# Kernel tuning notes

Hardware: AMD Instinct MI355X
Metric: run time of the kernel (lower is better)

The kernel has to match this reference:

```python
import jax, jax.numpy as jnp
import numpy as np

N_NODES = 122880  # 4096 graphs * 30 nodes
N_EDGES = 983040


def gcn_conv(x, W, b, src, dst, n):
    """PyG GCNConv: symmetric-normalized aggregation with self-loops."""
    h = x @ W  # [n, out]
    loop = jnp.arange(n, dtype=src.dtype)
    s = jnp.concatenate([src, loop])
    d = jnp.concatenate([dst, loop])
    deg = jnp.zeros((n,), dtype=h.dtype).at[d].add(1.0)  # >=1 due to self loops
    dinv = jax.lax.rsqrt(deg)
    norm = dinv[s] * dinv[d]  # [E+n]
    out = jax.ops.segment_sum(h[s] * norm[:, None], d, num_segments=n)
    return out + b


def setup_inputs() -> dict:
    key = jax.random.key(0)
    ks = jax.random.split(key, 8)
    x = jax.random.normal(ks[0], (N_NODES, 64), dtype=jnp.float32)
    edge_index = jax.random.randint(ks[1], (2, N_EDGES), 0, N_NODES, dtype=jnp.int64)
    W1 = jax.random.normal(ks[2], (64, 128), dtype=jnp.float32) * (1.0 / np.sqrt(64))
    b1 = jnp.zeros((128,), dtype=jnp.float32)
    W2 = jax.random.normal(ks[3], (128, 64), dtype=jnp.float32) * (1.0 / np.sqrt(128))
    b2 = jnp.zeros((64,), dtype=jnp.float32)
    Wfc = jax.random.normal(ks[4], (1920, 1728), dtype=jnp.float32) * (1.0 / np.sqrt(1920))
    bfc = jnp.zeros((1728,), dtype=jnp.float32)
    return {"x": x, "edge_index": edge_index, "W1": W1, "b1": b1,
            "W2": W2, "b2": b2, "Wfc": Wfc, "bfc": bfc}


def reference(x, edge_index, W1, b1, W2, b2, Wfc, bfc):
    n = x.shape[0]
    src, dst = edge_index[0], edge_index[1]
    h = gcn_conv(x, W1, b1, src, dst, n)
    h = jax.nn.relu(h)  # dropout is identity in eval mode
    h = gcn_conv(h, W2, b2, src, dst, n)
    h = jax.nn.relu(h)
    h = h.reshape(-1, 64 * 30)  # [B, 1920], 30 nodes per graph
    return h @ Wfc + bfc  # [B, 1728]
```

## Files before the change

kernel.cpp:

```cpp
#include <hip/hip_runtime.h>
#include <hip/hip_bf16.h>

#define N_NODES 122880
#define N_EDGES 983040
#define NBKT 480
#define BCAP 2560
#define EPB 4096
#define NPAD 1792

typedef __hip_bfloat16 bf16;
typedef __attribute__((ext_vector_type(8))) short short8;
typedef __attribute__((ext_vector_type(4))) float floatx4;

__device__ __forceinline__ void gl_lds16(const void* g, void* l) {
    __builtin_amdgcn_global_load_lds(
        (const __attribute__((address_space(1))) void*)g,
        (__attribute__((address_space(3))) void*)l, 16, 0, 0);
}

__device__ __forceinline__ float bflo(unsigned u) {
    return __uint_as_float(u << 16);
}
__device__ __forceinline__ float bfhi(unsigned u) {
    return __uint_as_float(u & 0xffff0000u);
}

__global__ __launch_bounds__(256) void k_psort_prep(
        const int* __restrict__ ei, int* __restrict__ gcur,
        unsigned* __restrict__ gbuf,
        const float* __restrict__ W1, const float* __restrict__ W2,
        const float* __restrict__ Wfc,
        bf16* __restrict__ W1T, bf16* __restrict__ W2T,
        bf16* __restrict__ WfcT) {
    __shared__ __align__(16) char smem[4352];
    const int b = blockIdx.x, t = threadIdx.x;
    if (b < 240) {
        int* cur = (int*)smem;
        int* gb  = (int*)(smem + 1920);
        for (int i = t; i < NBKT; i += 256) cur[i] = 0;
        __syncthreads();
        const int base = b * EPB;
        unsigned pay[16];
        short bk[16], pib[16];
#pragma unroll
        for (int j = 0; j < 16; ++j) {
            int e = base + j * 256 + t;
            int d = ei[N_EDGES + e];
            int s = ei[e];
            bk[j] = (short)(d >> 8);
            pay[j] = (unsigned)(d & 255) | ((unsigned)s << 8);
            pib[j] = (short)atomicAdd(&cur[d >> 8], 1);
        }
        __syncthreads();
        for (int i = t; i < NBKT; i += 256) {
            int c = cur[i];
            gb[i] = c ? atomicAdd(&gcur[i * 16], c) : 0;
        }
        __syncthreads();
#pragma unroll
        for (int j = 0; j < 16; ++j) {
            int pos = gb[bk[j]] + pib[j];
            if (pos < BCAP) gbuf[bk[j] * BCAP + pos] = pay[j];
        }
    } else if (b < 304) {
        int u = (b - 240) * 256 + t;
        if (u < 64 * 128) {
            int k = u >> 7, n = u & 127;
            W1T[n * 64 + k] = __float2bfloat16(W1[u]);
        } else {
            int v = u - 64 * 128;
            int k = v >> 6, n = v & 63;
            W2T[n * 128 + k] = __float2bfloat16(W2[v]);
        }
    } else {
        float (*ts)[33] = (float(*)[33])smem;
        const int bid2 = b - 304;
        const int n0 = (bid2 % 56) * 32, k0 = (bid2 / 56) * 32;
        const int tx = t & 31, ty = t >> 5;
        const bool nok = (n0 + tx) < 1728;
#pragma unroll
        for (int j = 0; j < 4; ++j)
            ts[ty + j * 8][tx] =
                nok ? Wfc[(long)(k0 + ty + j * 8) * 1728 + n0 + tx] : 0.0f;
        __syncthreads();
#pragma unroll
        for (int j = 0; j < 4; ++j)
            WfcT[(long)(n0 + ty + j * 8) * 1920 + k0 + tx] =
                __float2bfloat16(ts[tx][ty + j * 8]);
    }
}

__global__ __launch_bounds__(256) void k_bcsr(const int* __restrict__ gcur,
                                              const unsigned* __restrict__ gbuf,
                                              int* __restrict__ adj,
                                              unsigned* __restrict__ co,
                                              float* __restrict__ dinv,
                                              const float* __restrict__ x,
                                              bf16* __restrict__ xb) {
    __shared__ int hist[256];
    __shared__ int arr[256];
    __shared__ int exc[256];
    __shared__ float dinvs[256];
    const int b = blockIdx.x, t = threadIdx.x;
    hist[t] = 0;
    __syncthreads();
    int E = gcur[b * 16];
    if (E > BCAP) E = BCAP;
    int dl[10], sv[10];
    short pb[10];
    int n = 0;
    for (int idx = t; idx < E; idx += 256) {
        unsigned p = gbuf[b * BCAP + idx];
        dl[n] = p & 255;
        sv[n] = (int)(p >> 8);
        pb[n] = (short)atomicAdd(&hist[dl[n]], 1);
        ++n;
    }
    __syncthreads();
    const int cnt_t = hist[t];
    arr[t] = cnt_t;
    __syncthreads();
    for (int d = 1; d < 256; d <<= 1) {
        int v = (t >= d) ? arr[t - d] : 0;
        __syncthreads();
        arr[t] += v;
        __syncthreads();
    }
    const int ex = arr[t] - cnt_t;
    exc[t] = ex;
    const int node = b * 256 + t;
    co[node] = ((unsigned)ex << 16) | (unsigned)cnt_t;
    const float di = rsqrtf((float)cnt_t + 1.0f);
    dinv[node] = di;
    dinvs[t] = di;
    __syncthreads();
    for (int j = 0; j < n; ++j)
        adj[b * BCAP + exc[dl[j]] + pb[j]] = sv[j];

    const long xbase = (long)b * 256 * 64;
    for (int r = 0; r < 16; ++r) {
        int u = r * 256 + t;
        int nl = u >> 4;
        const float4 v = ((const float4*)(x + xbase))[u];
        const float d2 = dinvs[nl];
        bf16* o = xb + xbase + u * 4;
        o[0] = __float2bfloat16(d2 * v.x);
        o[1] = __float2bfloat16(d2 * v.y);
        o[2] = __float2bfloat16(d2 * v.z);
        o[3] = __float2bfloat16(d2 * v.w);
    }
}

template <bool BIAS_RELU>
__global__ __launch_bounds__(256) void k_agg(const bf16* __restrict__ xb,
                                             const float* __restrict__ dinv,
                                             const unsigned* __restrict__ co,
                                             const int* __restrict__ adj,
                                             const float* __restrict__ bias,
                                             bf16* __restrict__ out) {
    const int wave = threadIdx.x >> 6, lane = threadIdx.x & 63;
    const int sub = lane >> 4, l16 = lane & 15;
    const int node = blockIdx.x * 16 + wave * 4 + sub;

    const float di = dinv[node];
    const unsigned c_ = co[node];
    int c = (int)(c_ & 0xffffu);
    if (c > 32) c = 32;
    const int* al = adj + (node >> 8) * BCAP + (c_ >> 16);
    int sl  = (l16 < c)      ? al[l16]      : 0;
    int sl2 = (16 + l16 < c) ? al[16 + l16] : 0;

    const uint2 us = *(const uint2*)(xb + ((long)node << 6) + (l16 << 2));
    float a0 = bflo(us.x), a1 = bfhi(us.x);
    float a2 = bflo(us.y), a3 = bfhi(us.y);

    for (int p0 = 0; p0 < c; p0 += 8) {
        uint2 uu[8];
#pragma unroll
        for (int j = 0; j < 8; ++j) {
            int p = p0 + j;
            bool ok = p < c;
            int sv = (p < 16) ? sl : sl2;
            int s = __shfl(sv, p & 15, 16);
            uint2 u = *(const uint2*)(xb + ((long)s << 6) + (l16 << 2));
            uu[j].x = ok ? u.x : 0u;
            uu[j].y = ok ? u.y : 0u;
        }
#pragma unroll
        for (int j = 0; j < 8; ++j) {
            a0 += bflo(uu[j].x);
            a1 += bfhi(uu[j].x);
            a2 += bflo(uu[j].y);
            a3 += bfhi(uu[j].y);
        }
    }

    float r0 = di * a0, r1 = di * a1, r2 = di * a2, r3 = di * a3;
    if (BIAS_RELU) {
        r0 = fmaxf(r0 + bias[l16 * 4 + 0], 0.0f);
        r1 = fmaxf(r1 + bias[l16 * 4 + 1], 0.0f);
        r2 = fmaxf(r2 + bias[l16 * 4 + 2], 0.0f);
        r3 = fmaxf(r3 + bias[l16 * 4 + 3], 0.0f);
    }
    bf16* o = out + ((long)node << 6) + (l16 << 2);
    o[0] = __float2bfloat16(r0);
    o[1] = __float2bfloat16(r1);
    o[2] = __float2bfloat16(r2);
    o[3] = __float2bfloat16(r3);
}

__global__ __launch_bounds__(256) void k_mlp(const bf16* __restrict__ xa,
                                             const bf16* __restrict__ W1T,
                                             const bf16* __restrict__ W2T,
                                             const float* __restrict__ b1,
                                             const float* __restrict__ dinv,
                                             bf16* __restrict__ g) {
    __shared__ __align__(16) bf16 As[128 * 64];
    __shared__ __align__(16) bf16 C1s[128 * 136];
    const int tid = threadIdx.x;
    const int wave = tid >> 6, lane = tid & 63;
    const int quad = lane >> 4, l16 = lane & 15;
    const int bm = blockIdx.x * 128;
    const int wm = (wave & 1) * 64;
    const int wn1 = (wave >> 1) * 64;
    const int wn2 = (wave >> 1) * 32;

#pragma unroll
    for (int q = 0; q < 4; ++q) {
        int G = q * 256 + tid;
        int gc = (G & ~7) | ((G & 7) ^ ((G >> 3) & 7));
        gl_lds16(xa + (long)bm * 64 + gc * 8, As + ((q * 4 + wave) * 64) * 8);
    }
    short8 w1f[2][4];
#pragma unroll
    for (int kc = 0; kc < 2; ++kc)
#pragma unroll
        for (int in = 0; in < 4; ++in)
            w1f[kc][in] = *(const short8*)(W1T + (wn1 + in * 16 + l16) * 64 +
                                           kc * 32 + quad * 8);
    floatx4 acc1[4][4];
#pragma unroll
    for (int i = 0; i < 4; ++i)
#pragma unroll
        for (int j = 0; j < 4; ++j) acc1[i][j] = (floatx4){0.f, 0.f, 0.f, 0.f};
    __syncthreads();

#pragma unroll
    for (int kc = 0; kc < 2; ++kc)
#pragma unroll
        for (int im = 0; im < 4; ++im) {
            const int R = wm + im * 16 + l16;
            short8 af = *(const short8*)(As + R * 64 +
                                         (((kc * 4 + quad) ^ (R & 7)) * 8));
#pragma unroll
            for (int in = 0; in < 4; ++in)
                acc1[im][in] = __builtin_amdgcn_mfma_f32_16x16x32_bf16(
                    af, w1f[kc][in], acc1[im][in], 0, 0, 0);
        }

#pragma unroll
    for (int in = 0; in < 4; ++in) {
        const int col = wn1 + in * 16 + l16;
        const float bv = b1[col];
#pragma unroll
        for (int im = 0; im < 4; ++im) {
            const int row = wm + im * 16 + quad * 4;
#pragma unroll
            for (int r = 0; r < 4; ++r)
                C1s[(row + r) * 136 + col] =
                    __float2bfloat16(fmaxf(acc1[im][in][r] + bv, 0.0f));
        }
    }
    short8 w2f[4][2];
#pragma unroll
    for (int kc = 0; kc < 4; ++kc)
#pragma unroll
        for (int in = 0; in < 2; ++in)
            w2f[kc][in] = *(const short8*)(W2T + (wn2 + in * 16 + l16) * 128 +
                                           kc * 32 + quad * 8);
    floatx4 acc2[4][2];
#pragma unroll
    for (int i = 0; i < 4; ++i)
#pragma unroll
        for (int j = 0; j < 2; ++j) acc2[i][j] = (floatx4){0.f, 0.f, 0.f, 0.f};
    __syncthreads();

#pragma unroll
    for (int kc = 0; kc < 4; ++kc)
#pragma unroll
        for (int im = 0; im < 4; ++im) {
            short8 af = *(const short8*)(C1s + (wm + im * 16 + l16) * 136 +
                                         kc * 32 + quad * 8);
#pragma unroll
            for (int in = 0; in < 2; ++in)
                acc2[im][in] = __builtin_amdgcn_mfma_f32_16x16x32_bf16(
                    af, w2f[kc][in], acc2[im][in], 0, 0, 0);
        }

    float dv[4][4];
#pragma unroll
    for (int im = 0; im < 4; ++im)
#pragma unroll
        for (int r = 0; r < 4; ++r)
            dv[im][r] = dinv[bm + wm + im * 16 + quad * 4 + r];

#pragma unroll
    for (int in = 0; in < 2; ++in) {
        const int col = wn2 + in * 16 + l16;
#pragma unroll
        for (int im = 0; im < 4; ++im) {
            const int row = bm + wm + im * 16 + quad * 4;
#pragma unroll
            for (int r = 0; r < 4; ++r)
                g[(long)(row + r) * 64 + col] =
                    __float2bfloat16(dv[im][r] * acc2[im][in][r]);
        }
    }
}

template <bool RELU, bool BIAS, typename OutT>
__global__ __launch_bounds__(512) void gemm_bt(const bf16* __restrict__ A,
                                               const bf16* __restrict__ BT,
                                               const float* __restrict__ bias,
                                               OutT* __restrict__ C,
                                               int M, int N, int K) {
    __shared__ __align__(16) bf16 As[2][128 * 32];
    __shared__ __align__(16) bf16 Bs[2][128 * 32];
    const int tid = threadIdx.x;
    const int wave = tid >> 6, lane = tid & 63;
    const int quad = lane >> 4, l16 = lane & 15;
    const int bid = blockIdx.x;
    const int bx = (bid & 7) * 4 + ((bid >> 3) & 3);
    const int by = bid >> 5;
    const int bm = bx * 128, bn = by * 128;
    const int wm = (wave & 1) * 64, wn = (wave >> 1) * 32;

    floatx4 acc[4][2];
#pragma unroll
    for (int i = 0; i < 4; ++i)
#pragma unroll
        for (int j = 0; j < 2; ++j) acc[i][j] = (floatx4){0.f, 0.f, 0.f, 0.f};

    const int r4 = tid >> 2;
    const int cc = tid & 3;
    const int slot = r4 * 32 + ((cc ^ ((r4 >> 1) & 3)) * 8);

    const bf16* gA = A + (long)(bm + r4) * K + cc * 8;
    const bf16* gB = BT + (long)(bn + r4) * K + cc * 8;

    const int rsw = (l16 >> 1) & 3;
    const int NT = K >> 5;

    uint4 ra = *(const uint4*)gA;
    uint4 rb = *(const uint4*)gB;
    *(uint4*)(As[0] + slot) = ra;
    *(uint4*)(Bs[0] + slot) = rb;
    ra = *(const uint4*)(gA + 32);
    rb = *(const uint4*)(gB + 32);
    __syncthreads();

    for (int t = 0; t < NT; t += 2) {
        {
            short8 af[4], bfr[2];
#pragma unroll
            for (int im = 0; im < 4; ++im)
                af[im] = *(const short8*)(As[0] + (wm + im * 16 + l16) * 32 +
                                          (quad ^ rsw) * 8);
#pragma unroll
            for (int in = 0; in < 2; ++in)
                bfr[in] = *(const short8*)(Bs[0] + (wn + in * 16 + l16) * 32 +
                                           (quad ^ rsw) * 8);
            *(uint4*)(As[1] + slot) = ra;
            *(uint4*)(Bs[1] + slot) = rb;
            if (t + 2 < NT) {
                ra = *(const uint4*)(gA + (t + 2) * 32);
                rb = *(const uint4*)(gB + (t + 2) * 32);
            }
#pragma unroll
            for (int im = 0; im < 4; ++im)
#pragma unroll
                for (int in = 0; in < 2; ++in)
                    acc[im][in] = __builtin_amdgcn_mfma_f32_16x16x32_bf16(
                        af[im], bfr[in], acc[im][in], 0, 0, 0);
            __syncthreads();
        }
        {
            short8 af[4], bfr[2];
#pragma unroll
            for (int im = 0; im < 4; ++im)
                af[im] = *(const short8*)(As[1] + (wm + im * 16 + l16) * 32 +
                                          (quad ^ rsw) * 8);
#pragma unroll
            for (int in = 0; in < 2; ++in)
                bfr[in] = *(const short8*)(Bs[1] + (wn + in * 16 + l16) * 32 +
                                           (quad ^ rsw) * 8);
            if (t + 2 < NT) {
                *(uint4*)(As[0] + slot) = ra;
                *(uint4*)(Bs[0] + slot) = rb;
            }
            if (t + 3 < NT) {
                ra = *(const uint4*)(gA + (t + 3) * 32);
                rb = *(const uint4*)(gB + (t + 3) * 32);
            }
#pragma unroll
            for (int im = 0; im < 4; ++im)
#pragma unroll
                for (int in = 0; in < 2; ++in)
                    acc[im][in] = __builtin_amdgcn_mfma_f32_16x16x32_bf16(
                        af[im], bfr[in], acc[im][in], 0, 0, 0);
            __syncthreads();
        }
    }

#pragma unroll
    for (int in = 0; in < 2; ++in) {
        int gcol = bn + wn + in * 16 + l16;
        bool wok = gcol < N;
        float bv = (BIAS && wok) ? bias[gcol] : 0.0f;
#pragma unroll
        for (int im = 0; im < 4; ++im) {
            int mrow = bm + wm + im * 16 + quad * 4;
#pragma unroll
            for (int r = 0; r < 4; ++r) {
                float v = acc[im][in][r] + bv;
                if (RELU) v = fmaxf(v, 0.0f);
                if (wok) {
                    if constexpr (sizeof(OutT) == 2)
                        C[(long)(mrow + r) * N + gcol] = __float2bfloat16(v);
                    else
                        C[(long)(mrow + r) * N + gcol] = v;
                }
            }
        }
    }
}

extern "C" void kernel_launch(void* const* d_in, const int* in_sizes, int n_in,
                              void* d_out, int out_size, void* d_ws, size_t ws_size,
                              hipStream_t stream) {
    const float* x   = (const float*)d_in[0];
    const int*   ei  = (const int*)d_in[1];
    const float* W1  = (const float*)d_in[2];
    const float* b1  = (const float*)d_in[3];
    const float* W2  = (const float*)d_in[4];
    const float* b2  = (const float*)d_in[5];
    const float* Wfc = (const float*)d_in[6];
    const float* bfc = (const float*)d_in[7];

    char* p = (char*)d_ws;
    int*      gcur = (int*)p;      p += (size_t)NBKT * 16 * 4;
    unsigned* gbuf = (unsigned*)p; p += (size_t)NBKT * BCAP * 4;
    int*      adj  = (int*)p;      p += (size_t)NBKT * BCAP * 4;
    unsigned* co   = (unsigned*)p; p += (size_t)N_NODES * 4;
    float*    dinv = (float*)p;    p += (size_t)N_NODES * 4;
    bf16*     xb   = (bf16*)p;     p += (size_t)N_NODES * 64 * 2;
    bf16*     xa   = (bf16*)p;     p += (size_t)N_NODES * 64 * 2;
    bf16*     g    = (bf16*)p;     p += (size_t)N_NODES * 64 * 2;
    bf16*     h2   = (bf16*)p;     p += (size_t)N_NODES * 64 * 2;
    bf16*     W1T  = (bf16*)p;     p += 128 * 64 * 2;
    bf16*     W2T  = (bf16*)p;     p += 64 * 128 * 2;
    bf16*     WfcT = (bf16*)p;     p += (size_t)NPAD * 1920 * 2;

    hipMemsetAsync(gcur, 0, (size_t)NBKT * 16 * 4, stream);
    k_psort_prep<<<3664, 256, 0, stream>>>(ei, gcur, gbuf, W1, W2, Wfc,
                                           W1T, W2T, WfcT);
    k_bcsr<<<NBKT, 256, 0, stream>>>(gcur, gbuf, adj, co, dinv, x, xb);

    k_agg<false><<<N_NODES / 16, 256, 0, stream>>>(xb, dinv, co, adj, nullptr, xa);
    k_mlp<<<N_NODES / 128, 256, 0, stream>>>(xa, W1T, W2T, b1, dinv, g);
    k_agg<true><<<N_NODES / 16, 256, 0, stream>>>(g, dinv, co, adj, b2, h2);
    gemm_bt<false, true, float><<<448, 512, 0, stream>>>(
        h2, WfcT, bfc, (float*)d_out, 4096, 1728, 1920);
}
```

Baseline: 225.6 us.

## Fuse first-layer neighbor aggregation into the MLP kernel via LDS

Merges the first GCN aggregation kernel into the two-layer MLP kernel. Each block gathers neighbor features for its 128 nodes straight into a swizzled LDS tile instead of writing an intermediate bf16 buffer to global memory and reloading it. This removes one launch and a write plus read of a 122880x64 buffer. In exchange the grid shrinks from 7680 to 960 blocks, each block runs 8 serial gather passes, and the LDS-heavy kernel may keep fewer waves resident to hide the gather latency.

```diff
diff --git a/kernel.cpp b/kernel.cpp
--- a/kernel.cpp
+++ b/kernel.cpp
@@ -11,12 +11,6 @@
 typedef __hip_bfloat16 bf16;
 typedef __attribute__((ext_vector_type(8))) short short8;
 typedef __attribute__((ext_vector_type(4))) float floatx4;
-
-__device__ __forceinline__ void gl_lds16(const void* g, void* l) {
-    __builtin_amdgcn_global_load_lds(
-        (const __attribute__((address_space(1))) void*)g,
-        (__attribute__((address_space(3))) void*)l, 16, 0, 0);
-}
 
 __device__ __forceinline__ float bflo(unsigned u) {
     return __uint_as_float(u << 16);
@@ -151,6 +145,152 @@
     }
 }
 
+__global__ __launch_bounds__(256) void k_aggmlp(
+        const bf16* __restrict__ xb, const float* __restrict__ dinv,
+        const unsigned* __restrict__ co, const int* __restrict__ adj,
+        const bf16* __restrict__ W1T, const bf16* __restrict__ W2T,
+        const float* __restrict__ b1, bf16* __restrict__ g) {
+    __shared__ __align__(16) bf16 As[128 * 64];
+    __shared__ __align__(16) bf16 C1s[128 * 136];
+    const int tid = threadIdx.x;
+    const int wave = tid >> 6, lane = tid & 63;
+    const int quad = lane >> 4, l16 = lane & 15;
+    const int bm = blockIdx.x * 128;
+    const int wm = (wave & 1) * 64;
+    const int wn1 = (wave >> 1) * 64;
+    const int wn2 = (wave >> 1) * 32;
+
+    for (int p = 0; p < 8; ++p) {
+        const int r = p * 16 + wave * 4 + quad;
+        const int node = bm + r;
+        const float di = dinv[node];
+        const unsigned c_ = co[node];
+        int c = (int)(c_ & 0xffffu);
+        if (c > 32) c = 32;
+        const int* al = adj + (node >> 8) * BCAP + (c_ >> 16);
+        int sl  = (l16 < c)      ? al[l16]      : 0;
+        int sl2 = (16 + l16 < c) ? al[16 + l16] : 0;
+
+        const uint2 us = *(const uint2*)(xb + ((long)node << 6) + (l16 << 2));
+        float a0 = bflo(us.x), a1 = bfhi(us.x);
+        float a2 = bflo(us.y), a3 = bfhi(us.y);
+
+        for (int p0 = 0; p0 < c; p0 += 8) {
+            uint2 uu[8];
+#pragma unroll
+            for (int j = 0; j < 8; ++j) {
+                int pp = p0 + j;
+                bool ok = pp < c;
+                int sv = (pp < 16) ? sl : sl2;
+                int s = __shfl(sv, pp & 15, 16);
+                uint2 u = *(const uint2*)(xb + ((long)s << 6) + (l16 << 2));
+                uu[j].x = ok ? u.x : 0u;
+                uu[j].y = ok ? u.y : 0u;
+            }
+#pragma unroll
+            for (int j = 0; j < 8; ++j) {
+                a0 += bflo(uu[j].x);
+                a1 += bfhi(uu[j].x);
+                a2 += bflo(uu[j].y);
+                a3 += bfhi(uu[j].y);
+            }
+        }
+        ushort4 w;
+        w.x = __bfloat16_as_ushort(__float2bfloat16(di * a0));
+        w.y = __bfloat16_as_ushort(__float2bfloat16(di * a1));
+        w.z = __bfloat16_as_ushort(__float2bfloat16(di * a2));
+        w.w = __bfloat16_as_ushort(__float2bfloat16(di * a3));
+        *(ushort4*)(As + r * 64 + (((l16 >> 1) ^ (r & 7)) * 8) +
+                    (l16 & 1) * 4) = w;
+    }
+
+    short8 w1f[2][4];
+#pragma unroll
+    for (int kc = 0; kc < 2; ++kc)
+#pragma unroll
+        for (int in = 0; in < 4; ++in)
+            w1f[kc][in] = *(const short8*)(W1T + (wn1 + in * 16 + l16) * 64 +
+                                           kc * 32 + quad * 8);
+    floatx4 acc1[4][4];
+#pragma unroll
+    for (int i = 0; i < 4; ++i)
+#pragma unroll
+        for (int j = 0; j < 4; ++j) acc1[i][j] = (floatx4){0.f, 0.f, 0.f, 0.f};
+    __syncthreads();
+
+#pragma unroll
+    for (int kc = 0; kc < 2; ++kc)
+#pragma unroll
+        for (int im = 0; im < 4; ++im) {
+            const int R = wm + im * 16 + l16;
+            short8 af = *(const short8*)(As + R * 64 +
+                                         (((kc * 4 + quad) ^ (R & 7)) * 8));
+#pragma unroll
+            for (int in = 0; in < 4; ++in)
+                acc1[im][in] = __builtin_amdgcn_mfma_f32_16x16x32_bf16(
+                    af, w1f[kc][in], acc1[im][in], 0, 0, 0);
+        }
+
+#pragma unroll
+    for (int in = 0; in < 4; ++in) {
+        const int col = wn1 + in * 16 + l16;
+        const float bv = b1[col];
+#pragma unroll
+        for (int im = 0; im < 4; ++im) {
+            const int row = wm + im * 16 + quad * 4;
+#pragma unroll
+            for (int r = 0; r < 4; ++r)
+                C1s[(row + r) * 136 + col] =
+                    __float2bfloat16(fmaxf(acc1[im][in][r] + bv, 0.0f));
+        }
+    }
+    short8 w2f[4][2];
+#pragma unroll
+    for (int kc = 0; kc < 4; ++kc)
+#pragma unroll
+        for (int in = 0; in < 2; ++in)
+            w2f[kc][in] = *(const short8*)(W2T + (wn2 + in * 16 + l16) * 128 +
+                                           kc * 32 + quad * 8);
+    floatx4 acc2[4][2];
+#pragma unroll
+    for (int i = 0; i < 4; ++i)
+#pragma unroll
+        for (int j = 0; j < 2; ++j) acc2[i][j] = (floatx4){0.f, 0.f, 0.f, 0.f};
+    __syncthreads();
+
+#pragma unroll
+    for (int kc = 0; kc < 4; ++kc)
+#pragma unroll
+        for (int im = 0; im < 4; ++im) {
+            short8 af = *(const short8*)(C1s + (wm + im * 16 + l16) * 136 +
+                                         kc * 32 + quad * 8);
+#pragma unroll
+            for (int in = 0; in < 2; ++in)
+                acc2[im][in] = __builtin_amdgcn_mfma_f32_16x16x32_bf16(
+                    af, w2f[kc][in], acc2[im][in], 0, 0, 0);
+        }
+
+    float dv[4][4];
+#pragma unroll
+    for (int im = 0; im < 4; ++im)
+#pragma unroll
+        for (int r = 0; r < 4; ++r)
+            dv[im][r] = dinv[bm + wm + im * 16 + quad * 4 + r];
+
+#pragma unroll
+    for (int in = 0; in < 2; ++in) {
+        const int col = wn2 + in * 16 + l16;
+#pragma unroll
+        for (int im = 0; im < 4; ++im) {
+            const int row = bm + wm + im * 16 + quad * 4;
+#pragma unroll
+            for (int r = 0; r < 4; ++r)
+                g[(long)(row + r) * 64 + col] =
+                    __float2bfloat16(dv[im][r] * acc2[im][in][r]);
+        }
+    }
+}
+
 template <bool BIAS_RELU>
 __global__ __launch_bounds__(256) void k_agg(const bf16* __restrict__ xb,
                                              const float* __restrict__ dinv,
@@ -207,115 +347,6 @@
     o[1] = __float2bfloat16(r1);
     o[2] = __float2bfloat16(r2);
     o[3] = __float2bfloat16(r3);
-}
-
-__global__ __launch_bounds__(256) void k_mlp(const bf16* __restrict__ xa,
-                                             const bf16* __restrict__ W1T,
-                                             const bf16* __restrict__ W2T,
-                                             const float* __restrict__ b1,
-                                             const float* __restrict__ dinv,
-                                             bf16* __restrict__ g) {
-    __shared__ __align__(16) bf16 As[128 * 64];
-    __shared__ __align__(16) bf16 C1s[128 * 136];
-    const int tid = threadIdx.x;
-    const int wave = tid >> 6, lane = tid & 63;
-    const int quad = lane >> 4, l16 = lane & 15;
-    const int bm = blockIdx.x * 128;
-    const int wm = (wave & 1) * 64;
-    const int wn1 = (wave >> 1) * 64;
-    const int wn2 = (wave >> 1) * 32;
-
-#pragma unroll
-    for (int q = 0; q < 4; ++q) {
-        int G = q * 256 + tid;
-        int gc = (G & ~7) | ((G & 7) ^ ((G >> 3) & 7));
-        gl_lds16(xa + (long)bm * 64 + gc * 8, As + ((q * 4 + wave) * 64) * 8);
-    }
-    short8 w1f[2][4];
-#pragma unroll
-    for (int kc = 0; kc < 2; ++kc)
-#pragma unroll
-        for (int in = 0; in < 4; ++in)
-            w1f[kc][in] = *(const short8*)(W1T + (wn1 + in * 16 + l16) * 64 +
-                                           kc * 32 + quad * 8);
-    floatx4 acc1[4][4];
-#pragma unroll
-    for (int i = 0; i < 4; ++i)
-#pragma unroll
-        for (int j = 0; j < 4; ++j) acc1[i][j] = (floatx4){0.f, 0.f, 0.f, 0.f};
-    __syncthreads();
-
-#pragma unroll
-    for (int kc = 0; kc < 2; ++kc)
-#pragma unroll
-        for (int im = 0; im < 4; ++im) {
-            const int R = wm + im * 16 + l16;
-            short8 af = *(const short8*)(As + R * 64 +
-                                         (((kc * 4 + quad) ^ (R & 7)) * 8));
-#pragma unroll
-            for (int in = 0; in < 4; ++in)
-                acc1[im][in] = __builtin_amdgcn_mfma_f32_16x16x32_bf16(
-                    af, w1f[kc][in], acc1[im][in], 0, 0, 0);
-        }
-
-#pragma unroll
-    for (int in = 0; in < 4; ++in) {
-        const int col = wn1 + in * 16 + l16;
-        const float bv = b1[col];
-#pragma unroll
-        for (int im = 0; im < 4; ++im) {
-            const int row = wm + im * 16 + quad * 4;
-#pragma unroll
-            for (int r = 0; r < 4; ++r)
-                C1s[(row + r) * 136 + col] =
-                    __float2bfloat16(fmaxf(acc1[im][in][r] + bv, 0.0f));
-        }
-    }
-    short8 w2f[4][2];
-#pragma unroll
-    for (int kc = 0; kc < 4; ++kc)
-#pragma unroll
-        for (int in = 0; in < 2; ++in)
-            w2f[kc][in] = *(const short8*)(W2T + (wn2 + in * 16 + l16) * 128 +
-                                           kc * 32 + quad * 8);
-    floatx4 acc2[4][2];
-#pragma unroll
-    for (int i = 0; i < 4; ++i)
-#pragma unroll
-        for (int j = 0; j < 2; ++j) acc2[i][j] = (floatx4){0.f, 0.f, 0.f, 0.f};
-    __syncthreads();
-
-#pragma unroll
-    for (int kc = 0; kc < 4; ++kc)
-#pragma unroll
-        for (int im = 0; im < 4; ++im) {
-            short8 af = *(const short8*)(C1s + (wm + im * 16 + l16) * 136 +
-                                         kc * 32 + quad * 8);
-#pragma unroll
-            for (int in = 0; in < 2; ++in)
-                acc2[im][in] = __builtin_amdgcn_mfma_f32_16x16x32_bf16(
-                    af, w2f[kc][in], acc2[im][in], 0, 0, 0);
-        }
-
-    float dv[4][4];
-#pragma unroll
-    for (int im = 0; im < 4; ++im)
-#pragma unroll
-        for (int r = 0; r < 4; ++r)
-            dv[im][r] = dinv[bm + wm + im * 16 + quad * 4 + r];
-
-#pragma unroll
-    for (int in = 0; in < 2; ++in) {
-        const int col = wn2 + in * 16 + l16;
-#pragma unroll
-        for (int im = 0; im < 4; ++im) {
-            const int row = bm + wm + im * 16 + quad * 4;
-#pragma unroll
-            for (int r = 0; r < 4; ++r)
-                g[(long)(row + r) * 64 + col] =
-                    __float2bfloat16(dv[im][r] * acc2[im][in][r]);
-        }
-    }
 }
 
 template <bool RELU, bool BIAS, typename OutT>
@@ -454,7 +485,6 @@
     unsigned* co   = (unsigned*)p; p += (size_t)N_NODES * 4;
     float*    dinv = (float*)p;    p += (size_t)N_NODES * 4;
     bf16*     xb   = (bf16*)p;     p += (size_t)N_NODES * 64 * 2;
-    bf16*     xa   = (bf16*)p;     p += (size_t)N_NODES * 64 * 2;
     bf16*     g    = (bf16*)p;     p += (size_t)N_NODES * 64 * 2;
     bf16*     h2   = (bf16*)p;     p += (size_t)N_NODES * 64 * 2;
     bf16*     W1T  = (bf16*)p;     p += 128 * 64 * 2;
@@ -466,8 +496,8 @@
                                            W1T, W2T, WfcT);
     k_bcsr<<<NBKT, 256, 0, stream>>>(gcur, gbuf, adj, co, dinv, x, xb);
 
-    k_agg<false><<<N_NODES / 16, 256, 0, stream>>>(xb, dinv, co, adj, nullptr, xa);
-    k_mlp<<<N_NODES / 128, 256, 0, stream>>>(xa, W1T, W2T, b1, dinv, g);
+    k_aggmlp<<<N_NODES / 128, 256, 0, stream>>>(xb, dinv, co, adj,
+                                                W1T, W2T, b1, g);
     k_agg<true><<<N_NODES / 16, 256, 0, stream>>>(g, dinv, co, adj, b2, h2);
     gemm_bt<false, true, float><<<448, 512, 0, stream>>>(
         h2, WfcT, bfc, (float*)d_out, 4096, 1728, 1920);
```

Measured after the change: 233.9 us. +3.7%, slower.

## Replace global atomic bucket offsets with per-block segments and prefix scan

Applied to the files above, without the earlier changes.

The edge bucketing pass no longer uses global atomics on bucket cursors or a memset. Each sort block writes its edges into a fixed-capacity segment per bucket and records per-block counts. The CSR builder then prefix-scans those counts and binary-searches to locate each edge. This removes the memset, the global atomics and one barrier phase, and aliases the bucket buffer with the aggregation outputs to save workspace. In exchange it adds a scan and a per-edge binary search, and it silently drops edges if any block-bucket segment exceeds 40 entries.

```diff
diff --git a/kernel.cpp b/kernel.cpp
--- a/kernel.cpp
+++ b/kernel.cpp
@@ -6,6 +6,8 @@
 #define NBKT 480
 #define BCAP 2560
 #define EPB 4096
+#define NPB 240
+#define SEGCAP 40
 #define NPAD 1792
 
 typedef __hip_bfloat16 bf16;
@@ -26,7 +28,7 @@
 }
 
 __global__ __launch_bounds__(256) void k_psort_prep(
-        const int* __restrict__ ei, int* __restrict__ gcur,
+        const int* __restrict__ ei, unsigned short* __restrict__ cnt,
         unsigned* __restrict__ gbuf,
         const float* __restrict__ W1, const float* __restrict__ W2,
         const float* __restrict__ Wfc,
@@ -34,9 +36,8 @@
         bf16* __restrict__ WfcT) {
     __shared__ __align__(16) char smem[4352];
     const int b = blockIdx.x, t = threadIdx.x;
-    if (b < 240) {
+    if (b < NPB) {
         int* cur = (int*)smem;
-        int* gb  = (int*)(smem + 1920);
         for (int i = t; i < NBKT; i += 256) cur[i] = 0;
         __syncthreads();
         const int base = b * EPB;
@@ -51,19 +52,19 @@
             pay[j] = (unsigned)(d & 255) | ((unsigned)s << 8);
             pib[j] = (short)atomicAdd(&cur[d >> 8], 1);
         }
+#pragma unroll
+        for (int j = 0; j < 16; ++j) {
+            if (pib[j] < SEGCAP)
+                gbuf[((unsigned)bk[j] * NPB + b) * SEGCAP + pib[j]] = pay[j];
+        }
         __syncthreads();
         for (int i = t; i < NBKT; i += 256) {
             int c = cur[i];
-            gb[i] = c ? atomicAdd(&gcur[i * 16], c) : 0;
-        }
-        __syncthreads();
-#pragma unroll
-        for (int j = 0; j < 16; ++j) {
-            int pos = gb[bk[j]] + pib[j];
-            if (pos < BCAP) gbuf[bk[j] * BCAP + pos] = pay[j];
-        }
-    } else if (b < 304) {
-        int u = (b - 240) * 256 + t;
+            if (c > SEGCAP) c = SEGCAP;
+            cnt[i * NPB + b] = (unsigned short)c;
+        }
+    } else if (b < NPB + 64) {
+        int u = (b - NPB) * 256 + t;
         if (u < 64 * 128) {
             int k = u >> 7, n = u & 127;
             W1T[n * 64 + k] = __float2bfloat16(W1[u]);
@@ -74,7 +75,7 @@
         }
     } else {
         float (*ts)[33] = (float(*)[33])smem;
-        const int bid2 = b - 304;
+        const int bid2 = b - (NPB + 64);
         const int n0 = (bid2 % 56) * 32, k0 = (bid2 / 56) * 32;
         const int tx = t & 31, ty = t >> 5;
         const bool nok = (n0 + tx) < 1728;
@@ -90,27 +91,44 @@
     }
 }
 
-__global__ __launch_bounds__(256) void k_bcsr(const int* __restrict__ gcur,
-                                              const unsigned* __restrict__ gbuf,
-                                              int* __restrict__ adj,
-                                              unsigned* __restrict__ co,
-                                              float* __restrict__ dinv,
-                                              const float* __restrict__ x,
-                                              bf16* __restrict__ xb) {
+__global__ __launch_bounds__(256) void k_bcsr(
+        const unsigned short* __restrict__ cnt,
+        const unsigned* __restrict__ gbuf,
+        int* __restrict__ adj, unsigned* __restrict__ co,
+        float* __restrict__ dinv,
+        const float* __restrict__ x, bf16* __restrict__ xb) {
     __shared__ int hist[256];
     __shared__ int arr[256];
     __shared__ int exc[256];
+    __shared__ int soff[256];
     __shared__ float dinvs[256];
     const int b = blockIdx.x, t = threadIdx.x;
     hist[t] = 0;
-    __syncthreads();
-    int E = gcur[b * 16];
+
+    const int myc = (t < NPB) ? (int)cnt[b * NPB + t] : 0;
+    arr[t] = myc;
+    __syncthreads();
+    for (int d = 1; d < 256; d <<= 1) {
+        int v = (t >= d) ? arr[t - d] : 0;
+        __syncthreads();
+        arr[t] += v;
+        __syncthreads();
+    }
+    soff[t] = arr[t] - myc;
+    __syncthreads();
+    int E = arr[255];
     if (E > BCAP) E = BCAP;
+
     int dl[10], sv[10];
     short pb[10];
     int n = 0;
     for (int idx = t; idx < E; idx += 256) {
-        unsigned p = gbuf[b * BCAP + idx];
+        int lo = 0, hi = NPB - 1;
+        while (lo < hi) {
+            int mid = (lo + hi + 1) >> 1;
+            if (soff[mid] <= idx) lo = mid; else hi = mid - 1;
+        }
+        unsigned p = gbuf[((unsigned)b * NPB + lo) * SEGCAP + (idx - soff[lo])];
         dl[n] = p & 255;
         sv[n] = (int)(p >> 8);
         pb[n] = (short)atomicAdd(&hist[dl[n]], 1);
@@ -448,23 +466,25 @@
     const float* bfc = (const float*)d_in[7];
 
     char* p = (char*)d_ws;
-    int*      gcur = (int*)p;      p += (size_t)NBKT * 16 * 4;
-    unsigned* gbuf = (unsigned*)p; p += (size_t)NBKT * BCAP * 4;
+    unsigned short* cnt = (unsigned short*)p; p += (size_t)NBKT * NPB * 2;
     int*      adj  = (int*)p;      p += (size_t)NBKT * BCAP * 4;
     unsigned* co   = (unsigned*)p; p += (size_t)N_NODES * 4;
     float*    dinv = (float*)p;    p += (size_t)N_NODES * 4;
     bf16*     xb   = (bf16*)p;     p += (size_t)N_NODES * 64 * 2;
-    bf16*     xa   = (bf16*)p;     p += (size_t)N_NODES * 64 * 2;
-    bf16*     g    = (bf16*)p;     p += (size_t)N_NODES * 64 * 2;
+    char* uni = p;
+    unsigned* gbuf = (unsigned*)uni;
+    bf16*     xa   = (bf16*)uni;
+    bf16*     g    = (bf16*)(uni + (size_t)N_NODES * 64 * 2);
+    p = uni + 2 * (size_t)N_NODES * 64 * 2;
     bf16*     h2   = (bf16*)p;     p += (size_t)N_NODES * 64 * 2;
     bf16*     W1T  = (bf16*)p;     p += 128 * 64 * 2;
     bf16*     W2T  = (bf16*)p;     p += 64 * 128 * 2;
     bf16*     WfcT = (bf16*)p;     p += (size_t)NPAD * 1920 * 2;
 
-    hipMemsetAsync(gcur, 0, (size_t)NBKT * 16 * 4, stream);
-    k_psort_prep<<<3664, 256, 0, stream>>>(ei, gcur, gbuf, W1, W2, Wfc,
-                                           W1T, W2T, WfcT);
-    k_bcsr<<<NBKT, 256, 0, stream>>>(gcur, gbuf, adj, co, dinv, x, xb);
+    k_psort_prep<<<NPB + 64 + 3360, 256, 0, stream>>>(ei, cnt, gbuf,
+                                                      W1, W2, Wfc,
+                                                      W1T, W2T, WfcT);
+    k_bcsr<<<NBKT, 256, 0, stream>>>(cnt, gbuf, adj, co, dinv, x, xb);
 
     k_agg<false><<<N_NODES / 16, 256, 0, stream>>>(xb, dinv, co, adj, nullptr, xa);
     k_mlp<<<N_NODES / 128, 256, 0, stream>>>(xa, W1T, W2T, b1, dinv, g);
```

Measured after the change: 225.8 us. Within noise of the previous version (+0.1%).
